# Kernel tuning notes

Hardware: AMD Instinct MI355X
Metric: run time of the kernel (lower is better)

## Reference

```python
import jax, jax.numpy as jnp
import numpy as np

N = 50000
E = 800000
IN_DIM = 512
HID = 512
MLP_HID = 200
N_CLASSES = 2
BN_EPS = 1e-5


def setup_inputs() -> dict:
    key = jax.random.key(0)
    ks = jax.random.split(key, 12)
    def glorot(k, shape):
        fan_in, fan_out = shape[0], shape[1]
        lim = (6.0 / (fan_in + fan_out)) ** 0.5
        return jax.random.uniform(k, shape, jnp.float32, -lim, lim)
    return {
        "features": jax.random.normal(ks[0], (N, IN_DIM), jnp.float32),
        "src": jax.random.randint(ks[1], (E,), 0, N),
        "dst": jax.random.randint(ks[2], (E,), 0, N),
        # SAGEConv layer 1 & 2 (gcn aggregator -> only fc_neigh)
        "W1": glorot(ks[3], (IN_DIM, HID)),
        "b1": jnp.zeros((HID,), jnp.float32),
        "W2": glorot(ks[4], (HID, HID)),
        "b2": jnp.zeros((HID,), jnp.float32),
        # MLP predictor: Linear -> ReLU -> BatchNorm1d -> Linear
        "Wh": glorot(ks[5], (HID, MLP_HID)),
        "bh": jnp.zeros((MLP_HID,), jnp.float32),
        "gamma": jnp.ones((MLP_HID,), jnp.float32),
        "beta": jnp.zeros((MLP_HID,), jnp.float32),
        "Wo": glorot(ks[6], (MLP_HID, N_CLASSES)),
        "bo": jnp.zeros((N_CLASSES,), jnp.float32),
    }


def _sage_gcn_layer(h, src, dst, deg, W, b):
    # dgl.add_self_loop(g) + SAGEConv(aggregator_type='gcn'):
    # neigh_sum over (edges + self-loop) = segment_sum + h;
    # gcn aggregator then adds h_self once more and divides by (in_deg_with_selfloop + 1):
    #   h_neigh = (segment_sum(h[src]) + 2*h) / (deg_orig + 2)
    agg = jax.ops.segment_sum(h[src], dst, num_segments=h.shape[0])
    h_neigh = (agg + 2.0 * h) / (deg + 2.0)[:, None]
    # fc_neigh then activation=relu (fc commutes with the convex aggregation,
    # applied post-aggregation for clarity)
    return jax.nn.relu(h_neigh @ W + b)


def reference(features, src, dst, W1, b1, W2, b2, Wh, bh, gamma, beta, Wo, bo):
    n = features.shape[0]
    deg = jax.ops.segment_sum(jnp.ones_like(src, dtype=features.dtype), dst, num_segments=n)
    h = _sage_gcn_layer(features, src, dst, deg, W1, b1)  # dropout = identity (eval)
    h = _sage_gcn_layer(h, src, dst, deg, W2, b2)
    # MLP predictor (dropout identity): Linear -> ReLU -> BatchNorm1d -> Linear
    h = jax.nn.relu(h @ Wh + bh)
    mean = jnp.mean(h, axis=0)
    var = jnp.var(h, axis=0)  # biased var, matching torch BatchNorm training fwd
    h = (h - mean) * jax.lax.rsqrt(var + BN_EPS) * gamma + beta
    return h @ Wo + bo
```

## Files before the change

### kernel.cpp

```cpp
#include <hip/hip_runtime.h>

#define NN 50000
#define NE 800000
#define DIM 512
#define MLPH 200

typedef __attribute__((ext_vector_type(8))) short short8;
typedef __attribute__((ext_vector_type(4))) float f32x4;

__device__ inline unsigned short f2bf(float f) {
    unsigned int u = __float_as_uint(f);
    unsigned int r = (u + 0x7fffu + ((u >> 16) & 1u)) >> 16;
    return (unsigned short)r;
}
__device__ inline float bflo(unsigned u) { return __uint_as_float(u << 16); }
__device__ inline float bfhi(unsigned u) { return __uint_as_float(u & 0xffff0000u); }
__device__ inline unsigned pack2(float a, float b) {
    return (unsigned)f2bf(a) | ((unsigned)f2bf(b) << 16);
}

__global__ void k_hist(const int* __restrict__ dst, int* __restrict__ counts) {
    int e = blockIdx.x * blockDim.x + threadIdx.x;
    if (e < NE) atomicAdd(&counts[dst[e]], 1);
}

__global__ void k_part(const int* __restrict__ counts, int* __restrict__ partial) {
    int t = threadIdx.x;
    int i = blockIdx.x * 256 + t;
    int x = (i < NN) ? counts[i] : 0;
#pragma unroll
    for (int off = 32; off; off >>= 1) x += __shfl_down(x, off);
    __shared__ int ws[4];
    if ((t & 63) == 0) ws[t >> 6] = x;
    __syncthreads();
    if (t == 0) partial[blockIdx.x] = ws[0] + ws[1] + ws[2] + ws[3];
}

__global__ void k_scanp(int* __restrict__ partial, int* __restrict__ rowstart, int nb) {
    __shared__ int ws[4];
    int t = threadIdx.x;
    int x = (t < nb) ? partial[t] : 0;
    int v = x;
#pragma unroll
    for (int off = 1; off < 64; off <<= 1) {
        int u = __shfl_up(v, off);
        if ((t & 63) >= off) v += u;
    }
    if ((t & 63) == 63) ws[t >> 6] = v;
    __syncthreads();
    int add = 0;
#pragma unroll
    for (int w = 0; w < 4; w++)
        if (w < (t >> 6)) add += ws[w];
    if (t < nb) partial[t] = v - x + add;
    if (t == 255) rowstart[NN] = v + add;
}

__global__ void k_scan2(const int* __restrict__ counts, const int* __restrict__ pexcl,
                        int* __restrict__ rowstart, int* __restrict__ cursor) {
    __shared__ int ws[4];
    int t = threadIdx.x;
    int i = blockIdx.x * 256 + t;
    int x = (i < NN) ? counts[i] : 0;
    int v = x;
#pragma unroll
    for (int off = 1; off < 64; off <<= 1) {
        int u = __shfl_up(v, off);
        if ((t & 63) >= off) v += u;
    }
    if ((t & 63) == 63) ws[t >> 6] = v;
    __syncthreads();
    int add = 0;
#pragma unroll
    for (int w = 0; w < 4; w++)
        if (w < (t >> 6)) add += ws[w];
    if (i < NN) {
        int r = pexcl[blockIdx.x] + v - x + add;
        rowstart[i] = r;
        cursor[i] = r;
    }
}

__global__ void k_fill(const int* __restrict__ src, const int* __restrict__ dst,
                       int* __restrict__ cursor, int* __restrict__ adj) {
    int e = blockIdx.x * blockDim.x + threadIdx.x;
    if (e < NE) {
        int p = atomicAdd(&cursor[dst[e]], 1);
        adj[p] = src[e];
    }
}

__global__ void k_cvt(const float* __restrict__ in, ushort* __restrict__ out, int n4) {
    int i = blockIdx.x * blockDim.x + threadIdx.x;
    if (i >= n4) return;
    float4 v = *(const float4*)(in + (size_t)i * 4);
    ushort2 a{f2bf(v.x), f2bf(v.y)}, b{f2bf(v.z), f2bf(v.w)};
    *(ushort2*)(out + (size_t)i * 4) = a;
    *(ushort2*)(out + (size_t)i * 4 + 2) = b;
}

__global__ void k_wt3(const float* __restrict__ W1, const float* __restrict__ W2,
                      const float* __restrict__ Wh, ushort* __restrict__ W1t,
                      ushort* __restrict__ W2t, ushort* __restrict__ Wht) {
    int i = blockIdx.x * 256 + threadIdx.x;
    const int S1 = 512 * 512, S2 = 2 * 512 * 512, S3 = 2 * 512 * 512 + MLPH * 512;
    if (i < S1) {
        int n = i >> 9, k = i & 511;
        W1t[i] = f2bf(W1[(size_t)k * 512 + n]);
    } else if (i < S2) {
        int j = i - S1, n = j >> 9, k = j & 511;
        W2t[j] = f2bf(W2[(size_t)k * 512 + n]);
    } else if (i < S3) {
        int j = i - S2, n = j >> 9, k = j & 511;
        Wht[j] = f2bf(Wh[(size_t)k * MLPH + n]);
    }
}

__device__ inline void addrow(float* acc, uint4 v) {
    acc[0] += bflo(v.x); acc[1] += bfhi(v.x);
    acc[2] += bflo(v.y); acc[3] += bfhi(v.y);
    acc[4] += bflo(v.z); acc[5] += bfhi(v.z);
    acc[6] += bflo(v.w); acc[7] += bfhi(v.w);
}

__global__ __launch_bounds__(256) void k_agg_bf(const ushort* __restrict__ h,
                                                const int* __restrict__ rowstart,
                                                const int* __restrict__ adj,
                                                ushort* __restrict__ out) {
    int node = blockIdx.x * 4 + (threadIdx.x >> 6);
    int lane = threadIdx.x & 63;
    if (node >= NN) return;
    int s = rowstart[node], e = rowstart[node + 1];
    const size_t coff = (size_t)lane * 8;
    float acc[8];
    {
        uint4 v = *(const uint4*)(h + (size_t)node * DIM + coff);
        acc[0] = 2.f * bflo(v.x); acc[1] = 2.f * bfhi(v.x);
        acc[2] = 2.f * bflo(v.y); acc[3] = 2.f * bfhi(v.y);
        acc[4] = 2.f * bflo(v.z); acc[5] = 2.f * bfhi(v.z);
        acc[6] = 2.f * bflo(v.w); acc[7] = 2.f * bfhi(v.w);
    }
    int i = s;
    int e4 = s + ((e - s) & ~3);
    for (; i < e4; i += 4) {
        int n0 = adj[i], n1 = adj[i + 1], n2 = adj[i + 2], n3 = adj[i + 3];
        uint4 v0 = *(const uint4*)(h + (size_t)n0 * DIM + coff);
        uint4 v1 = *(const uint4*)(h + (size_t)n1 * DIM + coff);
        uint4 v2 = *(const uint4*)(h + (size_t)n2 * DIM + coff);
        uint4 v3 = *(const uint4*)(h + (size_t)n3 * DIM + coff);
        addrow(acc, v0);
        addrow(acc, v1);
        addrow(acc, v2);
        addrow(acc, v3);
    }
    for (; i < e; i++) {
        int nbr = adj[i];
        uint4 v = *(const uint4*)(h + (size_t)nbr * DIM + coff);
        addrow(acc, v);
    }
    float inv = 1.0f / (float)(e - s + 2);
    uint4 o;
    o.x = pack2(acc[0] * inv, acc[1] * inv);
    o.y = pack2(acc[2] * inv, acc[3] * inv);
    o.z = pack2(acc[4] * inv, acc[5] * inv);
    o.w = pack2(acc[6] * inv, acc[7] * inv);
    *(uint4*)(out + (size_t)node * DIM + coff) = o;
}

template <int NCOLS, bool OUT_BF16>
__global__ __launch_bounds__(256) void k_mgemm(const ushort* __restrict__ A,
                                               const ushort* __restrict__ Bt,
                                               const float* __restrict__ bias,
                                               float* __restrict__ Cf,
                                               ushort* __restrict__ Cb, int M) {
    constexpr int K = 512;
    constexpr int LDT = 40;
    __shared__ ushort As[128 * LDT];
    __shared__ ushort Bs[128 * LDT];
    const int tid = threadIdx.x;
    const int wid = tid >> 6, lane = tid & 63;
    const int wm = wid >> 1, wn = wid & 1;
    const int row0 = blockIdx.x * 128, col0 = blockIdx.y * 128;
    const int srow = tid >> 2;
    const int sq = tid & 3;
    const int l15 = lane & 15, lk = (lane >> 4) * 8;

    f32x4 acc[4][4] = {};
    uint4 va[2], vb[2];

    auto loadAB = [&](int k0, uint4* a, uint4* b) {
#pragma unroll
        for (int half = 0; half < 2; half++) {
            int r = srow + half * 64;
            int gr = row0 + r;
            a[half] = uint4{0, 0, 0, 0};
            if (gr < M) a[half] = *(const uint4*)(A + (size_t)gr * K + k0 + sq * 8);
            int gc = col0 + r;
            b[half] = uint4{0, 0, 0, 0};
            if (NCOLS % 128 == 0 || gc < NCOLS)
                b[half] = *(const uint4*)(Bt + (size_t)gc * K + k0 + sq * 8);
        }
    };

    loadAB(0, va, vb);
    for (int k0 = 0; k0 < K; k0 += 32) {
        __syncthreads();
#pragma unroll
        for (int half = 0; half < 2; half++) {
            int r = srow + half * 64;
            *(uint4*)(As + r * LDT + sq * 8) = va[half];
            *(uint4*)(Bs + r * LDT + sq * 8) = vb[half];
        }
        uint4 na[2], nb[2];
        if (k0 + 32 < K) loadAB(k0 + 32, na, nb);
        __syncthreads();
        short8 a[4], b[4];
#pragma unroll
        for (int m = 0; m < 4; m++)
            a[m] = *(const short8*)(As + (wm * 64 + m * 16 + l15) * LDT + lk);
#pragma unroll
        for (int n = 0; n < 4; n++)
            b[n] = *(const short8*)(Bs + (wn * 64 + n * 16 + l15) * LDT + lk);
#pragma unroll
        for (int m = 0; m < 4; m++)
#pragma unroll
            for (int n = 0; n < 4; n++)
                acc[m][n] = __builtin_amdgcn_mfma_f32_16x16x32_bf16(a[m], b[n], acc[m][n], 0, 0, 0);
        if (k0 + 32 < K) {
#pragma unroll
            for (int half = 0; half < 2; half++) {
                va[half] = na[half];
                vb[half] = nb[half];
            }
        }
    }

    const int crow = row0 + wm * 64;
    const int ccol = col0 + wn * 64;
#pragma unroll
    for (int n = 0; n < 4; n++) {
        int c = ccol + n * 16 + l15;
        if (NCOLS % 128 != 0 && c >= NCOLS) continue;
        float bv = bias[c];
#pragma unroll
        for (int m = 0; m < 4; m++) {
#pragma unroll
            for (int i = 0; i < 4; i++) {
                int r = crow + m * 16 + (lane >> 4) * 4 + i;
                if (r >= M) continue;
                float v = fmaxf(acc[m][n][i] + bv, 0.0f);
                if (OUT_BF16) Cb[(size_t)r * NCOLS + c] = f2bf(v);
                else Cf[(size_t)r * NCOLS + c] = v;
            }
        }
    }
}

__global__ void k_bnstat(const float* __restrict__ hm, float* __restrict__ gsum,
                         float* __restrict__ gsq) {
    int j = threadIdx.x;
    if (j >= MLPH) return;
    float s = 0.f, q = 0.f;
    for (int r = blockIdx.x; r < NN; r += gridDim.x) {
        float v = hm[(size_t)r * MLPH + j];
        s += v;
        q += v * v;
    }
    atomicAdd(&gsum[j], s);
    atomicAdd(&gsq[j], q);
}

__global__ void k_bnfin(const float* __restrict__ gsum, const float* __restrict__ gsq,
                        const float* __restrict__ gamma, const float* __restrict__ beta,
                        const float* __restrict__ Wo, const float* __restrict__ bo,
                        float* __restrict__ Wo2, float* __restrict__ bo2) {
    __shared__ float sh[MLPH];
    int j = threadIdx.x;
    if (j < MLPH) {
        float mean = gsum[j] / (float)NN;
        float var = gsq[j] / (float)NN - mean * mean;
        float scale = gamma[j] * rsqrtf(var + 1e-5f);
        float shift = beta[j] - mean * scale;
        sh[j] = shift;
        Wo2[j * 2 + 0] = scale * Wo[j * 2 + 0];
        Wo2[j * 2 + 1] = scale * Wo[j * 2 + 1];
    }
    __syncthreads();
    if (j < 2) {
        float acc = bo[j];
        for (int t = 0; t < MLPH; t++) acc += sh[t] * Wo[t * 2 + j];
        bo2[j] = acc;
    }
}

__global__ void k_out(const float* __restrict__ hm, const float* __restrict__ Wo2,
                      const float* __restrict__ bo2, float* __restrict__ out) {
    __shared__ float w[MLPH * 2];
    if (threadIdx.x < MLPH * 2) w[threadIdx.x] = Wo2[threadIdx.x];
    __syncthreads();
    int wid = (blockIdx.x * blockDim.x + threadIdx.x) >> 6;
    int lane = threadIdx.x & 63;
    if (wid >= NN) return;
    const float* row = hm + (size_t)wid * MLPH;
    float p0 = 0.f, p1 = 0.f;
    for (int j = lane; j < MLPH; j += 64) {
        float v = row[j];
        p0 += v * w[j * 2 + 0];
        p1 += v * w[j * 2 + 1];
    }
    for (int off = 32; off; off >>= 1) {
        p0 += __shfl_down(p0, off);
        p1 += __shfl_down(p1, off);
    }
    if (lane == 0) {
        out[wid * 2 + 0] = p0 + bo2[0];
        out[wid * 2 + 1] = p1 + bo2[1];
    }
}

extern "C" void kernel_launch(void* const* d_in, const int* in_sizes, int n_in,
                              void* d_out, int out_size, void* d_ws, size_t ws_size,
                              hipStream_t stream) {
    const float* features = (const float*)d_in[0];
    const int* src = (const int*)d_in[1];
    const int* dst = (const int*)d_in[2];
    const float* W1 = (const float*)d_in[3];
    const float* b1 = (const float*)d_in[4];
    const float* W2 = (const float*)d_in[5];
    const float* b2 = (const float*)d_in[6];
    const float* Wh = (const float*)d_in[7];
    const float* bh = (const float*)d_in[8];
    const float* gamma = (const float*)d_in[9];
    const float* beta = (const float*)d_in[10];
    const float* Wo = (const float*)d_in[11];
    const float* bo = (const float*)d_in[12];
    float* out = (float*)d_out;

    char* w = (char*)d_ws;
    auto alloc = [&](size_t bytes) -> void* {
        void* p = (void*)w;
        w += (bytes + 255) & ~(size_t)255;
        return p;
    };
    ushort* fb = (ushort*)alloc((size_t)NN * DIM * 2);
    ushort* ab = (ushort*)alloc((size_t)NN * DIM * 2);
    ushort* hb = (ushort*)alloc((size_t)NN * DIM * 2);
    float* hm = (float*)alloc((size_t)NN * MLPH * 4);
    ushort* W1t = (ushort*)alloc((size_t)DIM * DIM * 2);
    ushort* W2t = (ushort*)alloc((size_t)DIM * DIM * 2);
    ushort* Wht = (ushort*)alloc((size_t)MLPH * DIM * 2);
    int* adj = (int*)alloc((size_t)NE * 4);
    int* counts = (int*)alloc((size_t)NN * 4);
    int* rowstart = (int*)alloc((size_t)(NN + 1) * 4);
    int* cursor = (int*)alloc((size_t)NN * 4);
    int* partial = (int*)alloc(256 * 4);
    float* gsum = (float*)alloc(MLPH * 4);
    float* gsq = (float*)alloc(MLPH * 4);
    float* Wo2 = (float*)alloc(MLPH * 2 * 4);
    float* bo2 = (float*)alloc(2 * 4);

    hipMemsetAsync(counts, 0, (size_t)NN * 4, stream);
    hipMemsetAsync(gsum, 0, MLPH * 4, stream);
    hipMemsetAsync(gsq, 0, MLPH * 4, stream);

    const int NB = (NN + 255) / 256;

    k_hist<<<(NE + 255) / 256, 256, 0, stream>>>(dst, counts);
    k_part<<<NB, 256, 0, stream>>>(counts, partial);
    k_scanp<<<1, 256, 0, stream>>>(partial, rowstart, NB);
    k_scan2<<<NB, 256, 0, stream>>>(counts, partial, rowstart, cursor);
    k_fill<<<(NE + 255) / 256, 256, 0, stream>>>(src, dst, cursor, adj);

    const int n4 = NN * DIM / 4;
    k_cvt<<<(n4 + 255) / 256, 256, 0, stream>>>(features, fb, n4);
    const int WT = 2 * 512 * 512 + MLPH * 512;
    k_wt3<<<(WT + 255) / 256, 256, 0, stream>>>(W1, W2, Wh, W1t, W2t, Wht);

    const int MB = (NN + 127) / 128;

    k_agg_bf<<<(NN + 3) / 4, 256, 0, stream>>>(fb, rowstart, adj, ab);
    k_mgemm<DIM, true><<<dim3(MB, DIM / 128), 256, 0, stream>>>(ab, W1t, b1, nullptr, hb, NN);
    k_agg_bf<<<(NN + 3) / 4, 256, 0, stream>>>(hb, rowstart, adj, ab);
    k_mgemm<DIM, true><<<dim3(MB, DIM / 128), 256, 0, stream>>>(ab, W2t, b2, nullptr, fb, NN);
    k_mgemm<MLPH, false><<<dim3(MB, 2), 256, 0, stream>>>(fb, Wht, bh, hm, nullptr, NN);
    k_bnstat<<<512, 256, 0, stream>>>(hm, gsum, gsq);
    k_bnfin<<<1, 256, 0, stream>>>(gsum, gsq, gamma, beta, Wo, bo, Wo2, bo2);
    k_out<<<(NN * 64 + 511) / 512, 512, 0, stream>>>(hm, Wo2, bo2, out);
}
```

Baseline: 630.5 us.

## Store aggregation inputs in column-sliced layout for cache-local neighbor gathers

Node features feeding the neighbor aggregation are now stored as 16 column slices of 32 bf16 values per node, written by the conversion kernel and by the first GEMM epilogue. The aggregation kernel runs one grid dimension per slice, with 8 lanes per node reading 8 bytes each. The goal is to shrink the working set of each slice pass (50000×64 bytes) so random neighbor gathers hit in L2/MALL instead of DRAM. In exchange, the adjacency list is read 16 times, gathers become smaller, and the GEMM epilogue writes to scattered addresses.

```diff
diff --git a/kernel.cpp b/kernel.cpp
--- a/kernel.cpp
+++ b/kernel.cpp
@@ -4,6 +4,8 @@
 #define NE 800000
 #define DIM 512
 #define MLPH 200
+#define SCOLS 32
+#define NSLICE (DIM / SCOLS)
 
 typedef __attribute__((ext_vector_type(8))) short short8;
 typedef __attribute__((ext_vector_type(4))) float f32x4;
@@ -90,13 +92,16 @@
     }
 }
 
-__global__ void k_cvt(const float* __restrict__ in, ushort* __restrict__ out, int n4) {
-    int i = blockIdx.x * blockDim.x + threadIdx.x;
-    if (i >= n4) return;
-    float4 v = *(const float4*)(in + (size_t)i * 4);
-    ushort2 a{f2bf(v.x), f2bf(v.y)}, b{f2bf(v.z), f2bf(v.w)};
-    *(ushort2*)(out + (size_t)i * 4) = a;
-    *(ushort2*)(out + (size_t)i * 4 + 2) = b;
+__global__ void k_cvt_sl(const float* __restrict__ in, ushort* __restrict__ out) {
+    int i = blockIdx.x * 256 + threadIdx.x;
+    if (i >= NN * (DIM / 4)) return;
+    int n = i >> 7, cu = i & 127;
+    int c = cu * 4;
+    float4 v = *(const float4*)(in + (size_t)n * DIM + c);
+    uint2 o;
+    o.x = pack2(v.x, v.y);
+    o.y = pack2(v.z, v.w);
+    *(uint2*)(out + ((size_t)(c >> 5) * NN + n) * SCOLS + (c & 31)) = o;
 }
 
 __global__ void k_wt3(const float* __restrict__ W1, const float* __restrict__ W2,
@@ -116,58 +121,55 @@
     }
 }
 
-__device__ inline void addrow(float* acc, uint4 v) {
-    acc[0] += bflo(v.x); acc[1] += bfhi(v.x);
-    acc[2] += bflo(v.y); acc[3] += bfhi(v.y);
-    acc[4] += bflo(v.z); acc[5] += bfhi(v.z);
-    acc[6] += bflo(v.w); acc[7] += bfhi(v.w);
-}
-
-__global__ __launch_bounds__(256) void k_agg_bf(const ushort* __restrict__ h,
+__global__ __launch_bounds__(256) void k_agg_sl(const ushort* __restrict__ hs,
                                                 const int* __restrict__ rowstart,
                                                 const int* __restrict__ adj,
                                                 ushort* __restrict__ out) {
-    int node = blockIdx.x * 4 + (threadIdx.x >> 6);
-    int lane = threadIdx.x & 63;
-    if (node >= NN) return;
-    int s = rowstart[node], e = rowstart[node + 1];
-    const size_t coff = (size_t)lane * 8;
-    float acc[8];
+    const int slice = blockIdx.y;
+    const int wid = threadIdx.x >> 6;
+    const int lane = threadIdx.x & 63;
+    const int g = lane >> 3;
+    const int sub = lane & 7;
+    int node = blockIdx.x * 32 + wid * 8 + g;
+    const bool valid = node < NN;
+    const int nd = valid ? node : 0;
+    const int s = rowstart[nd], e = rowstart[nd + 1];
+    const ushort* base = hs + (size_t)slice * NN * SCOLS + sub * 4;
+
+    float a0, a1, a2, a3;
     {
-        uint4 v = *(const uint4*)(h + (size_t)node * DIM + coff);
-        acc[0] = 2.f * bflo(v.x); acc[1] = 2.f * bfhi(v.x);
-        acc[2] = 2.f * bflo(v.y); acc[3] = 2.f * bfhi(v.y);
-        acc[4] = 2.f * bflo(v.z); acc[5] = 2.f * bfhi(v.z);
-        acc[6] = 2.f * bflo(v.w); acc[7] = 2.f * bfhi(v.w);
+        uint2 v = *(const uint2*)(base + (size_t)nd * SCOLS);
+        a0 = 2.f * bflo(v.x);
+        a1 = 2.f * bfhi(v.x);
+        a2 = 2.f * bflo(v.y);
+        a3 = 2.f * bfhi(v.y);
     }
     int i = s;
-    int e4 = s + ((e - s) & ~3);
-    for (; i < e4; i += 4) {
-        int n0 = adj[i], n1 = adj[i + 1], n2 = adj[i + 2], n3 = adj[i + 3];
-        uint4 v0 = *(const uint4*)(h + (size_t)n0 * DIM + coff);
-        uint4 v1 = *(const uint4*)(h + (size_t)n1 * DIM + coff);
-        uint4 v2 = *(const uint4*)(h + (size_t)n2 * DIM + coff);
-        uint4 v3 = *(const uint4*)(h + (size_t)n3 * DIM + coff);
-        addrow(acc, v0);
-        addrow(acc, v1);
-        addrow(acc, v2);
-        addrow(acc, v3);
-    }
-    for (; i < e; i++) {
-        int nbr = adj[i];
-        uint4 v = *(const uint4*)(h + (size_t)nbr * DIM + coff);
-        addrow(acc, v);
-    }
-    float inv = 1.0f / (float)(e - s + 2);
-    uint4 o;
-    o.x = pack2(acc[0] * inv, acc[1] * inv);
-    o.y = pack2(acc[2] * inv, acc[3] * inv);
-    o.z = pack2(acc[4] * inv, acc[5] * inv);
-    o.w = pack2(acc[6] * inv, acc[7] * inv);
-    *(uint4*)(out + (size_t)node * DIM + coff) = o;
-}
-
-template <int NCOLS, bool OUT_BF16>
+    for (; i + 1 < e; i += 2) {
+        int n0 = adj[i], n1 = adj[i + 1];
+        uint2 v0 = *(const uint2*)(base + (size_t)n0 * SCOLS);
+        uint2 v1 = *(const uint2*)(base + (size_t)n1 * SCOLS);
+        a0 += bflo(v0.x); a1 += bfhi(v0.x);
+        a2 += bflo(v0.y); a3 += bfhi(v0.y);
+        a0 += bflo(v1.x); a1 += bfhi(v1.x);
+        a2 += bflo(v1.y); a3 += bfhi(v1.y);
+    }
+    if (i < e) {
+        int n0 = adj[i];
+        uint2 v0 = *(const uint2*)(base + (size_t)n0 * SCOLS);
+        a0 += bflo(v0.x); a1 += bfhi(v0.x);
+        a2 += bflo(v0.y); a3 += bfhi(v0.y);
+    }
+    if (valid) {
+        float inv = 1.0f / (float)(e - s + 2);
+        uint2 o;
+        o.x = pack2(a0 * inv, a1 * inv);
+        o.y = pack2(a2 * inv, a3 * inv);
+        *(uint2*)(out + (size_t)node * DIM + slice * SCOLS + sub * 4) = o;
+    }
+}
+
+template <int NCOLS, int OMODE>
 __global__ __launch_bounds__(256) void k_mgemm(const ushort* __restrict__ A,
                                                const ushort* __restrict__ Bt,
                                                const float* __restrict__ bias,
@@ -249,8 +251,9 @@
                 int r = crow + m * 16 + (lane >> 4) * 4 + i;
                 if (r >= M) continue;
                 float v = fmaxf(acc[m][n][i] + bv, 0.0f);
-                if (OUT_BF16) Cb[(size_t)r * NCOLS + c] = f2bf(v);
-                else Cf[(size_t)r * NCOLS + c] = v;
+                if (OMODE == 0) Cf[(size_t)r * NCOLS + c] = v;
+                else if (OMODE == 1) Cb[(size_t)r * NCOLS + c] = f2bf(v);
+                else Cb[((size_t)(c >> 5) * NN + r) * SCOLS + (c & 31)] = f2bf(v);
             }
         }
     }
@@ -371,18 +374,19 @@
     k_scan2<<<NB, 256, 0, stream>>>(counts, partial, rowstart, cursor);
     k_fill<<<(NE + 255) / 256, 256, 0, stream>>>(src, dst, cursor, adj);
 
-    const int n4 = NN * DIM / 4;
-    k_cvt<<<(n4 + 255) / 256, 256, 0, stream>>>(features, fb, n4);
+    const int ncu = NN * (DIM / 4);
+    k_cvt_sl<<<(ncu + 255) / 256, 256, 0, stream>>>(features, fb);
     const int WT = 2 * 512 * 512 + MLPH * 512;
     k_wt3<<<(WT + 255) / 256, 256, 0, stream>>>(W1, W2, Wh, W1t, W2t, Wht);
 
     const int MB = (NN + 127) / 128;
-
-    k_agg_bf<<<(NN + 3) / 4, 256, 0, stream>>>(fb, rowstart, adj, ab);
-    k_mgemm<DIM, true><<<dim3(MB, DIM / 128), 256, 0, stream>>>(ab, W1t, b1, nullptr, hb, NN);
-    k_agg_bf<<<(NN + 3) / 4, 256, 0, stream>>>(hb, rowstart, adj, ab);
-    k_mgemm<DIM, true><<<dim3(MB, DIM / 128), 256, 0, stream>>>(ab, W2t, b2, nullptr, fb, NN);
-    k_mgemm<MLPH, false><<<dim3(MB, 2), 256, 0, stream>>>(fb, Wht, bh, hm, nullptr, NN);
+    const dim3 AG((NN + 31) / 32, NSLICE);
+
+    k_agg_sl<<<AG, 256, 0, stream>>>(fb, rowstart, adj, ab);
+    k_mgemm<DIM, 2><<<dim3(MB, DIM / 128), 256, 0, stream>>>(ab, W1t, b1, nullptr, hb, NN);
+    k_agg_sl<<<AG, 256, 0, stream>>>(hb, rowstart, adj, ab);
+    k_mgemm<DIM, 1><<<dim3(MB, DIM / 128), 256, 0, stream>>>(ab, W2t, b2, nullptr, fb, NN);
+    k_mgemm<MLPH, 0><<<dim3(MB, 2), 256, 0, stream>>>(fb, Wht, bh, hm, nullptr, NN);
     k_bnstat<<<512, 256, 0, stream>>>(hm, gsum, gsq);
     k_bnfin<<<1, 256, 0, stream>>>(gsum, gsq, gamma, beta, Wo, bo, Wo2, bo2);
     k_out<<<(NN * 64 + 511) / 512, 512, 0, stream>>>(hm, Wo2, bo2, out);
```

Result: slower. 668.7 us (+6.1%).

## Add full-K A-tile resident GEMM kernel for 512-wide SAGE layers

Applied to the files above, without the earlier changes.

Replaces the 4-column-block GEMM grid for the two 512x512 layers with a kernel that loads a 128x512 row tile of A into LDS once and sweeps all 512 output columns in two 256-wide chunks with 8 waves. Each A row is then read from global memory once instead of four times. The cost is a large LDS footprint of about 150 KB per block, which limits occupancy, and an unpipelined upfront A load. The original templated kernel is narrowed to the fp32-output MLP GEMM.

```diff
diff --git a/kernel.cpp b/kernel.cpp
--- a/kernel.cpp
+++ b/kernel.cpp
@@ -167,12 +167,91 @@
     *(uint4*)(out + (size_t)node * DIM + coff) = o;
 }
 
-template <int NCOLS, bool OUT_BF16>
+__global__ __launch_bounds__(512) void k_gemm512(const ushort* __restrict__ A,
+                                                 const ushort* __restrict__ Bt,
+                                                 const float* __restrict__ bias,
+                                                 ushort* __restrict__ C, int M) {
+    constexpr int K = 512;
+    constexpr int LDA = 520;
+    constexpr int LDB = 40;
+    __shared__ ushort As[128 * LDA];
+    __shared__ ushort Bs[256 * LDB];
+    const int tid = threadIdx.x;
+    const int row0 = blockIdx.x * 128;
+
+    {
+        const int r = tid >> 2;
+        const int q = tid & 3;
+        const int gr = row0 + r;
+        const bool ok = gr < M;
+        const ushort* srcp = A + (size_t)gr * K + q * 8;
+#pragma unroll
+        for (int kk = 0; kk < 16; kk++) {
+            uint4 v = ok ? *(const uint4*)(srcp + kk * 32) : uint4{0, 0, 0, 0};
+            *(uint4*)(As + r * LDA + q * 8 + kk * 32) = v;
+        }
+    }
+
+    const int wid = tid >> 6, lane = tid & 63;
+    const int wm = wid >> 2;
+    const int wn = wid & 3;
+    const int l15 = lane & 15, lk = (lane >> 4) * 8;
+    const int bcol = tid >> 1;
+    const int bseg = (tid & 1) * 16;
+
+#pragma unroll
+    for (int ch = 0; ch < 2; ch++) {
+        const int col0 = ch * 256;
+        f32x4 acc[4][4] = {};
+        const ushort* bsrc = Bt + (size_t)(col0 + bcol) * K + bseg;
+        uint4 pb0 = *(const uint4*)(bsrc);
+        uint4 pb1 = *(const uint4*)(bsrc + 8);
+        for (int k0 = 0; k0 < K; k0 += 32) {
+            __syncthreads();
+            *(uint4*)(Bs + bcol * LDB + bseg) = pb0;
+            *(uint4*)(Bs + bcol * LDB + bseg + 8) = pb1;
+            __syncthreads();
+            if (k0 + 32 < K) {
+                pb0 = *(const uint4*)(bsrc + k0 + 32);
+                pb1 = *(const uint4*)(bsrc + k0 + 32 + 8);
+            }
+            short8 a[4], b[4];
+#pragma unroll
+            for (int m = 0; m < 4; m++)
+                a[m] = *(const short8*)(As + (wm * 64 + m * 16 + l15) * LDA + k0 + lk);
+#pragma unroll
+            for (int n = 0; n < 4; n++)
+                b[n] = *(const short8*)(Bs + (wn * 64 + n * 16 + l15) * LDB + lk);
+#pragma unroll
+            for (int m = 0; m < 4; m++)
+#pragma unroll
+                for (int n = 0; n < 4; n++)
+                    acc[m][n] = __builtin_amdgcn_mfma_f32_16x16x32_bf16(a[m], b[n], acc[m][n], 0, 0, 0);
+        }
+        const int crow = row0 + wm * 64;
+        const int ccol = col0 + wn * 64;
+#pragma unroll
+        for (int n = 0; n < 4; n++) {
+            int c = ccol + n * 16 + l15;
+            float bv = bias[c];
+#pragma unroll
+            for (int m = 0; m < 4; m++) {
+#pragma unroll
+                for (int i = 0; i < 4; i++) {
+                    int r = crow + m * 16 + (lane >> 4) * 4 + i;
+                    if (r >= M) continue;
+                    C[(size_t)r * 512 + c] = f2bf(fmaxf(acc[m][n][i] + bv, 0.0f));
+                }
+            }
+        }
+    }
+}
+
+template <int NCOLS>
 __global__ __launch_bounds__(256) void k_mgemm(const ushort* __restrict__ A,
                                                const ushort* __restrict__ Bt,
                                                const float* __restrict__ bias,
-                                               float* __restrict__ Cf,
-                                               ushort* __restrict__ Cb, int M) {
+                                               float* __restrict__ Cf, int M) {
     constexpr int K = 512;
     constexpr int LDT = 40;
     __shared__ ushort As[128 * LDT];
@@ -197,8 +276,7 @@
             if (gr < M) a[half] = *(const uint4*)(A + (size_t)gr * K + k0 + sq * 8);
             int gc = col0 + r;
             b[half] = uint4{0, 0, 0, 0};
-            if (NCOLS % 128 == 0 || gc < NCOLS)
-                b[half] = *(const uint4*)(Bt + (size_t)gc * K + k0 + sq * 8);
+            if (gc < NCOLS) b[half] = *(const uint4*)(Bt + (size_t)gc * K + k0 + sq * 8);
         }
     };
 
@@ -240,7 +318,7 @@
 #pragma unroll
     for (int n = 0; n < 4; n++) {
         int c = ccol + n * 16 + l15;
-        if (NCOLS % 128 != 0 && c >= NCOLS) continue;
+        if (c >= NCOLS) continue;
         float bv = bias[c];
 #pragma unroll
         for (int m = 0; m < 4; m++) {
@@ -248,9 +326,7 @@
             for (int i = 0; i < 4; i++) {
                 int r = crow + m * 16 + (lane >> 4) * 4 + i;
                 if (r >= M) continue;
-                float v = fmaxf(acc[m][n][i] + bv, 0.0f);
-                if (OUT_BF16) Cb[(size_t)r * NCOLS + c] = f2bf(v);
-                else Cf[(size_t)r * NCOLS + c] = v;
+                Cf[(size_t)r * NCOLS + c] = fmaxf(acc[m][n][i] + bv, 0.0f);
             }
         }
     }
@@ -379,10 +455,10 @@
     const int MB = (NN + 127) / 128;
 
     k_agg_bf<<<(NN + 3) / 4, 256, 0, stream>>>(fb, rowstart, adj, ab);
-    k_mgemm<DIM, true><<<dim3(MB, DIM / 128), 256, 0, stream>>>(ab, W1t, b1, nullptr, hb, NN);
+    k_gemm512<<<MB, 512, 0, stream>>>(ab, W1t, b1, hb, NN);
     k_agg_bf<<<(NN + 3) / 4, 256, 0, stream>>>(hb, rowstart, adj, ab);
-    k_mgemm<DIM, true><<<dim3(MB, DIM / 128), 256, 0, stream>>>(ab, W2t, b2, nullptr, fb, NN);
-    k_mgemm<MLPH, false><<<dim3(MB, 2), 256, 0, stream>>>(fb, Wht, bh, hm, nullptr, NN);
+    k_gemm512<<<MB, 512, 0, stream>>>(ab, W2t, b2, fb, NN);
+    k_mgemm<MLPH><<<dim3(MB, 2), 256, 0, stream>>>(fb, Wht, bh, hm, NN);
     k_bnstat<<<512, 256, 0, stream>>>(hm, gsum, gsq);
     k_bnfin<<<1, 256, 0, stream>>>(gsum, gsq, gamma, beta, Wo, bo, Wo2, bo2);
     k_out<<<(NN * 64 + 511) / 512, 512, 0, stream>>>(hm, Wo2, bo2, out);
```

Result: slower. 646.2 us (+2.5%).

## Stage GEMM tiles with direct global-to-LDS loads and double buffering

Applied to the files above, without the earlier changes.

The bf16 MFMA GEMM now loads A and B tiles straight into shared memory with global_load_lds, using two LDS buffers. This removes the register staging and cuts the barriers per k-step from two to one. The grid is swapped so blocks sharing a row tile launch next to each other, which improves L2 reuse of the A rows. LDS rows are no longer padded, so the MFMA operand reads may hit bank conflicts, and out-of-range rows are clamped rather than zero-filled.

```diff
diff --git a/kernel.cpp b/kernel.cpp
--- a/kernel.cpp
+++ b/kernel.cpp
@@ -7,6 +7,11 @@
 
 typedef __attribute__((ext_vector_type(8))) short short8;
 typedef __attribute__((ext_vector_type(4))) float f32x4;
+
+#define GL2LDS(g, l)                                                     \
+    __builtin_amdgcn_global_load_lds(                                    \
+        (const __attribute__((address_space(1))) unsigned int*)(g),      \
+        (__attribute__((address_space(3))) unsigned int*)(l), 16, 0, 0)
 
 __device__ inline unsigned short f2bf(float f) {
     unsigned int u = __float_as_uint(f);
@@ -167,72 +172,61 @@
     *(uint4*)(out + (size_t)node * DIM + coff) = o;
 }
 
-template <int NCOLS, bool OUT_BF16>
-__global__ __launch_bounds__(256) void k_mgemm(const ushort* __restrict__ A,
+template <int NCOLS, int OMODE>
+__global__ __launch_bounds__(256) void k_ggemm(const ushort* __restrict__ A,
                                                const ushort* __restrict__ Bt,
                                                const float* __restrict__ bias,
                                                float* __restrict__ Cf,
                                                ushort* __restrict__ Cb, int M) {
     constexpr int K = 512;
-    constexpr int LDT = 40;
-    __shared__ ushort As[128 * LDT];
-    __shared__ ushort Bs[128 * LDT];
+    constexpr int NT = K / 32;
+    __shared__ ushort As[2][128 * 32];
+    __shared__ ushort Bs[2][128 * 32];
     const int tid = threadIdx.x;
     const int wid = tid >> 6, lane = tid & 63;
     const int wm = wid >> 1, wn = wid & 1;
-    const int row0 = blockIdx.x * 128, col0 = blockIdx.y * 128;
-    const int srow = tid >> 2;
-    const int sq = tid & 3;
+    const int col0 = blockIdx.x * 128;
+    const int row0 = blockIdx.y * 128;
     const int l15 = lane & 15, lk = (lane >> 4) * 8;
 
-    f32x4 acc[4][4] = {};
-    uint4 va[2], vb[2];
-
-    auto loadAB = [&](int k0, uint4* a, uint4* b) {
-#pragma unroll
-        for (int half = 0; half < 2; half++) {
-            int r = srow + half * 64;
-            int gr = row0 + r;
-            a[half] = uint4{0, 0, 0, 0};
-            if (gr < M) a[half] = *(const uint4*)(A + (size_t)gr * K + k0 + sq * 8);
-            int gc = col0 + r;
-            b[half] = uint4{0, 0, 0, 0};
-            if (NCOLS % 128 == 0 || gc < NCOLS)
-                b[half] = *(const uint4*)(Bt + (size_t)gc * K + k0 + sq * 8);
+    const int sbase = wid * 32;
+    const int lrow = lane >> 2;
+    const int lseg = (lane & 3) * 8;
+
+    auto stage = [&](int buf, int k0) {
+#pragma unroll
+        for (int j = 0; j < 2; j++) {
+            const int r = sbase + j * 16;
+            int gr = row0 + r + lrow;
+            if (gr > M - 1) gr = M - 1;
+            GL2LDS(A + (size_t)gr * K + k0 + lseg, &As[buf][r * 32]);
+            int gc = col0 + r + lrow;
+            if (NCOLS % 128 != 0) {
+                if (gc > NCOLS - 1) gc = NCOLS - 1;
+            }
+            GL2LDS(Bt + (size_t)gc * K + k0 + lseg, &Bs[buf][r * 32]);
         }
     };
 
-    loadAB(0, va, vb);
-    for (int k0 = 0; k0 < K; k0 += 32) {
-        __syncthreads();
-#pragma unroll
-        for (int half = 0; half < 2; half++) {
-            int r = srow + half * 64;
-            *(uint4*)(As + r * LDT + sq * 8) = va[half];
-            *(uint4*)(Bs + r * LDT + sq * 8) = vb[half];
-        }
-        uint4 na[2], nb[2];
-        if (k0 + 32 < K) loadAB(k0 + 32, na, nb);
-        __syncthreads();
+    f32x4 acc[4][4] = {};
+    stage(0, 0);
+    __syncthreads();
+    for (int t = 0; t < NT; ++t) {
+        const int cur = t & 1;
+        if (t + 1 < NT) stage(cur ^ 1, (t + 1) * 32);
         short8 a[4], b[4];
 #pragma unroll
         for (int m = 0; m < 4; m++)
-            a[m] = *(const short8*)(As + (wm * 64 + m * 16 + l15) * LDT + lk);
+            a[m] = *(const short8*)(&As[cur][(wm * 64 + m * 16 + l15) * 32 + lk]);
 #pragma unroll
         for (int n = 0; n < 4; n++)
-            b[n] = *(const short8*)(Bs + (wn * 64 + n * 16 + l15) * LDT + lk);
+            b[n] = *(const short8*)(&Bs[cur][(wn * 64 + n * 16 + l15) * 32 + lk]);
 #pragma unroll
         for (int m = 0; m < 4; m++)
 #pragma unroll
             for (int n = 0; n < 4; n++)
                 acc[m][n] = __builtin_amdgcn_mfma_f32_16x16x32_bf16(a[m], b[n], acc[m][n], 0, 0, 0);
-        if (k0 + 32 < K) {
-#pragma unroll
-            for (int half = 0; half < 2; half++) {
-                va[half] = na[half];
-                vb[half] = nb[half];
-            }
-        }
+        __syncthreads();
     }
 
     const int crow = row0 + wm * 64;
@@ -249,8 +243,8 @@
                 int r = crow + m * 16 + (lane >> 4) * 4 + i;
                 if (r >= M) continue;
                 float v = fmaxf(acc[m][n][i] + bv, 0.0f);
-                if (OUT_BF16) Cb[(size_t)r * NCOLS + c] = f2bf(v);
-                else Cf[(size_t)r * NCOLS + c] = v;
+                if (OMODE == 0) Cf[(size_t)r * NCOLS + c] = v;
+                else Cb[(size_t)r * NCOLS + c] = f2bf(v);
             }
         }
     }
@@ -379,10 +373,10 @@
     const int MB = (NN + 127) / 128;
 
     k_agg_bf<<<(NN + 3) / 4, 256, 0, stream>>>(fb, rowstart, adj, ab);
-    k_mgemm<DIM, true><<<dim3(MB, DIM / 128), 256, 0, stream>>>(ab, W1t, b1, nullptr, hb, NN);
+    k_ggemm<DIM, 1><<<dim3(4, MB), 256, 0, stream>>>(ab, W1t, b1, nullptr, hb, NN);
     k_agg_bf<<<(NN + 3) / 4, 256, 0, stream>>>(hb, rowstart, adj, ab);
-    k_mgemm<DIM, true><<<dim3(MB, DIM / 128), 256, 0, stream>>>(ab, W2t, b2, nullptr, fb, NN);
-    k_mgemm<MLPH, false><<<dim3(MB, 2), 256, 0, stream>>>(fb, Wht, bh, hm, nullptr, NN);
+    k_ggemm<DIM, 1><<<dim3(4, MB), 256, 0, stream>>>(ab, W2t, b2, nullptr, fb, NN);
+    k_ggemm<MLPH, 0><<<dim3(2, MB), 256, 0, stream>>>(fb, Wht, bh, hm, nullptr, NN);
     k_bnstat<<<512, 256, 0, stream>>>(hm, gsum, gsq);
     k_bnfin<<<1, 256, 0, stream>>>(gsum, gsq, gamma, beta, Wo, bo, Wo2, bo2);
     k_out<<<(NN * 64 + 511) / 512, 512, 0, stream>>>(hm, Wo2, bo2, out);
```

New measurement: 604.4 us, median of 2. 4.1% less time.
